# Optimization experiments

Measured on AMD Instinct MI355X. Metric: run time of the kernel, lower is better.

## Reference

```python
import jax, jax.numpy as jnp
import numpy as np

N_NODES = 50000
N_EDGES = 800000
IN_CH = 1024
OUT_CH = 256


def setup_inputs() -> dict:
    key = jax.random.key(0)
    ks = jax.random.split(key, 7)
    x = jax.random.normal(ks[0], (N_NODES, IN_CH), dtype=jnp.float32)
    src_index = jax.random.randint(ks[1], (N_EDGES,), 0, N_NODES, dtype=jnp.int32)
    tar_index = jax.random.randint(ks[2], (N_EDGES,), 0, N_NODES, dtype=jnp.int32)
    edge_weight = jax.random.uniform(ks[3], (N_EDGES,), dtype=jnp.float32)
    self_edge_weight = jax.random.uniform(ks[4], (N_NODES,), dtype=jnp.float32)
    # Linear layer params (torch.nn.Linear: y = x @ W.T + b)
    bound = 1.0 / np.sqrt(IN_CH)
    W = jax.random.uniform(ks[5], (OUT_CH, IN_CH), dtype=jnp.float32, minval=-bound, maxval=bound)
    b = jax.random.uniform(ks[6], (OUT_CH,), dtype=jnp.float32, minval=-bound, maxval=bound)
    return {"x": x, "W": W, "b": b, "src_index": src_index, "tar_index": tar_index,
            "edge_weight": edge_weight, "self_edge_weight": self_edge_weight}


def reference(x, W, b, src_index, tar_index, edge_weight, self_edge_weight):
    # dense linear projection: [N, in] -> [N, out]
    h = jnp.einsum('ni,oi->no', x, W) + b
    # edge aggregation: out[t] += w_e * h[src_e]  (SpMM-like gather/scatter)
    msgs = h[src_index] * edge_weight[:, None]          # [E, out]
    agg = jax.ops.segment_sum(msgs, tar_index, num_segments=h.shape[0])
    # self-loop term
    return agg + self_edge_weight[:, None] * h
```

## Files before the change

kernel.cpp:

```cpp
#include <hip/hip_runtime.h>
#include <hip/hip_bf16.h>

#define N_NODES 50000
#define N_EDGES 800000
#define IN_CH 1024
#define OUT_CH 256
#define NBLK 196

typedef __attribute__((ext_vector_type(8))) short bf16x8;
typedef __attribute__((ext_vector_type(4))) float f32x4;

__device__ inline unsigned short f2bf(float f) {
  union { float f; unsigned int u; } v; v.f = f;
  unsigned int r = v.u + 0x7fffu + ((v.u >> 16) & 1u);
  return (unsigned short)(r >> 16);
}
__device__ inline float bf2f(unsigned short u) {
  union { unsigned int u; float f; } v; v.u = ((unsigned int)u) << 16;
  return v.f;
}
__device__ inline unsigned int cvtpk_bf16(float a, float b) {
  unsigned int r;
  asm("v_cvt_pk_bf16_f32 %0, %1, %2" : "=v"(r) : "v"(a), "v"(b));
  return r;
}

#define GLOAD16(SRC, DST)                                                      \
  __builtin_amdgcn_global_load_lds(                                            \
      (const __attribute__((address_space(1))) void*)(SRC),                    \
      (__attribute__((address_space(3))) void*)(DST), 16, 0, 0)

__device__ inline void waitbar6() {
  __builtin_amdgcn_sched_barrier(0);
  asm volatile("s_waitcnt vmcnt(6)" ::: "memory");
  __builtin_amdgcn_s_barrier();
  __builtin_amdgcn_sched_barrier(0);
}
__device__ inline void waitbar0() {
  __builtin_amdgcn_sched_barrier(0);
  asm volatile("s_waitcnt vmcnt(0)" ::: "memory");
  __builtin_amdgcn_s_barrier();
  __builtin_amdgcn_sched_barrier(0);
}

__global__ __launch_bounds__(256) void prep_hist(const float* __restrict__ W,
                                                 unsigned short* __restrict__ Wb,
                                                 const int* __restrict__ tar,
                                                 int* __restrict__ counts) {
  const int b = blockIdx.x, t = threadIdx.x;
  if (b < 256) {
    const int i4 = (b * 256 + t) * 4;
    float4 f = *(const float4*)(W + i4);
    *(ushort4*)(Wb + i4) = make_ushort4(f2bf(f.x), f2bf(f.y), f2bf(f.z), f2bf(f.w));
  } else {
    const int e = (b - 256) * 256 + t;
    if (e < N_EDGES) atomicAdd(&counts[tar[e]], 1);
  }
}

__global__ __launch_bounds__(256, 2) void gemm_proj(
    const float* __restrict__ X, const unsigned short* __restrict__ Wb,
    const float* __restrict__ bias, unsigned short* __restrict__ Hb)
{
  __shared__ float lds_a[3][128][32];
  __shared__ unsigned short lds_b[3][128][32];

  const int tid  = threadIdx.x;
  const int lane = tid & 63;
  const int w    = tid >> 6;
  const int wr   = w >> 1, wc = w & 1;
  const int gm0  = blockIdx.x * 128;
  const int gn0  = blockIdx.y * 128;

  f32x4 acc[4][4];
  #pragma unroll
  for (int i = 0; i < 4; i++)
    #pragma unroll
    for (int j = 0; j < 4; j++) acc[i][j] = (f32x4)0.0f;

#define STAGE(BUF, K0)                                                         \
  {                                                                            \
    _Pragma("unroll")                                                          \
    for (int q = 0; q < 4; q++) {                                              \
      const int wl  = w * 4 + q;                                               \
      const int row = 8 * wl + (lane >> 3);                                    \
      int grow = gm0 + row;                                                    \
      if (grow > N_NODES - 1) grow = N_NODES - 1;                              \
      const int sc = (lane & 7) ^ (row & 7);                                   \
      GLOAD16(X + (size_t)grow * IN_CH + (K0) + sc * 4,                        \
              &lds_a[BUF][8 * wl][0]);                                         \
    }                                                                          \
    _Pragma("unroll")                                                          \
    for (int q = 0; q < 2; q++) {                                              \
      const int wl  = w * 2 + q;                                               \
      const int row = 16 * wl + (lane >> 2);                                   \
      const int sc  = (lane & 3) ^ (row & 3);                                  \
      GLOAD16(Wb + (size_t)(gn0 + row) * IN_CH + (K0) + sc * 8,                \
              &lds_b[BUF][16 * wl][0]);                                        \
    }                                                                          \
  }

#define COMPUTE(BUF)                                                           \
  {                                                                            \
    const int l15 = lane & 15;                                                 \
    const int kb  = lane >> 4;                                                 \
    bf16x8 af[4], bfr[4];                                                      \
    _Pragma("unroll")                                                          \
    for (int i = 0; i < 4; i++) {                                              \
      const int row = wr * 64 + i * 16 + l15;                                  \
      const int c0  = (2 * kb) ^ (row & 7);                                    \
      const int c1  = (2 * kb + 1) ^ (row & 7);                                \
      f32x4 lo = *(const f32x4*)&lds_a[BUF][row][c0 * 4];                      \
      f32x4 hi = *(const f32x4*)&lds_a[BUF][row][c1 * 4];                      \
      union { unsigned int u[4]; bf16x8 v; } t;                                \
      t.u[0] = cvtpk_bf16(lo[0], lo[1]);                                       \
      t.u[1] = cvtpk_bf16(lo[2], lo[3]);                                       \
      t.u[2] = cvtpk_bf16(hi[0], hi[1]);                                       \
      t.u[3] = cvtpk_bf16(hi[2], hi[3]);                                       \
      af[i] = t.v;                                                             \
    }                                                                          \
    _Pragma("unroll")                                                          \
    for (int j = 0; j < 4; j++) {                                              \
      const int row = wc * 64 + j * 16 + l15;                                  \
      const int c   = kb ^ (row & 3);                                          \
      bfr[j] = *(const bf16x8*)&lds_b[BUF][row][c * 8];                        \
    }                                                                          \
    _Pragma("unroll")                                                          \
    for (int i = 0; i < 4; i++)                                                \
      _Pragma("unroll")                                                        \
      for (int j = 0; j < 4; j++)                                              \
        acc[i][j] = __builtin_amdgcn_mfma_f32_16x16x32_bf16(af[i], bfr[j],     \
                                                            acc[i][j], 0, 0, 0); \
  }

  STAGE(0, 0);
  STAGE(1, 32);
  waitbar6();

  #pragma unroll
  for (int t = 0; t < 32; t++) {
    if (t + 2 < 32) STAGE((t + 2) % 3, (t + 2) * 32);
    COMPUTE(t % 3);
    if (t + 2 < 32)      waitbar6();
    else if (t == 30)    waitbar0();
  }
#undef STAGE
#undef COMPUTE

  float bj[4];
  #pragma unroll
  for (int j = 0; j < 4; j++)
    bj[j] = bias[gn0 + wc * 64 + j * 16 + (lane & 15)];

  #pragma unroll
  for (int i = 0; i < 4; i++) {
    const int grow_base = gm0 + wr * 64 + i * 16 + ((lane >> 4) << 2);
    #pragma unroll
    for (int r = 0; r < 4; r++) {
      const int grow = grow_base + r;
      if (grow < N_NODES) {
        #pragma unroll
        for (int j = 0; j < 4; j++) {
          const int gcol = gn0 + wc * 64 + j * 16 + (lane & 15);
          Hb[(size_t)grow * OUT_CH + gcol] = f2bf(acc[i][j][r] + bj[j]);
        }
      }
    }
  }
}

__global__ __launch_bounds__(256) void scan_block(const int* __restrict__ counts,
                                                  int* __restrict__ offsets,
                                                  int* __restrict__ blocksum) {
  __shared__ int wsum[4];
  const int tid = threadIdx.x, lane = tid & 63, wv = tid >> 6;
  const int i = blockIdx.x * 256 + tid;
  const int v = (i < N_NODES) ? counts[i] : 0;
  int s = v;
  #pragma unroll
  for (int off = 1; off < 64; off <<= 1) {
    int t = __shfl_up(s, off, 64);
    if (lane >= off) s += t;
  }
  if (lane == 63) wsum[wv] = s;
  __syncthreads();
  if (tid == 0) {
    int c = 0;
    #pragma unroll
    for (int k = 0; k < 4; k++) { int t = wsum[k]; wsum[k] = c; c += t; }
  }
  __syncthreads();
  const int excl = wsum[wv] + s - v;
  if (i < N_NODES) offsets[i] = excl;
  if (tid == 255) blocksum[blockIdx.x] = excl + v;
}

__global__ __launch_bounds__(256) void scan_sums(int* __restrict__ blocksum,
                                                 int* __restrict__ offsets) {
  __shared__ int wsum[4];
  const int tid = threadIdx.x, lane = tid & 63, wv = tid >> 6;
  const int v = (tid < NBLK) ? blocksum[tid] : 0;
  int s = v;
  #pragma unroll
  for (int off = 1; off < 64; off <<= 1) {
    int t = __shfl_up(s, off, 64);
    if (lane >= off) s += t;
  }
  if (lane == 63) wsum[wv] = s;
  __syncthreads();
  if (tid == 0) {
    int c = 0;
    #pragma unroll
    for (int k = 0; k < 4; k++) { int t = wsum[k]; wsum[k] = c; c += t; }
  }
  __syncthreads();
  const int excl = wsum[wv] + s - v;
  if (tid < NBLK) blocksum[tid] = excl;
  if (tid == 255) offsets[N_NODES] = excl;
}

__global__ __launch_bounds__(256) void finalize_offsets(int* __restrict__ offsets,
                                                        const int* __restrict__ blocksum,
                                                        int* __restrict__ cursor) {
  const int i = blockIdx.x * 256 + threadIdx.x;
  if (i < N_NODES) {
    const int off = offsets[i] + blocksum[i >> 8];
    offsets[i] = off;
    cursor[i] = off;
  }
}

__global__ __launch_bounds__(256) void fill_csr(const int* __restrict__ src,
                                                const int* __restrict__ tar,
                                                const float* __restrict__ ew,
                                                int* __restrict__ cursor,
                                                int2* __restrict__ edata) {
  int e = blockIdx.x * blockDim.x + threadIdx.x;
  if (e >= N_EDGES) return;
  const int t = tar[e];
  const int p = atomicAdd(&cursor[t], 1);
  edata[p] = make_int2(src[e], __float_as_int(ew[e]));
}

__global__ __launch_bounds__(256) void node_agg(
    const unsigned short* __restrict__ Hb, const int* __restrict__ offsets,
    const int2* __restrict__ edata, const float* __restrict__ sw,
    float* __restrict__ OUT)
{
  const int wid = (blockIdx.x * blockDim.x + threadIdx.x) >> 6;
  if (wid >= N_NODES) return;
  const int lane = threadIdx.x & 63;
  const int e0 = offsets[wid];
  const int e1 = offsets[wid + 1];

  float a0 = 0.f, a1 = 0.f, a2 = 0.f, a3 = 0.f;

  for (int base = e0; base < e1; base += 64) {
    const int avail = e1 - base;
    int2 d = make_int2(0, 0);
    if (lane < avail) d = edata[base + lane];
    const int n = (avail < 64) ? avail : 64;
    int j = 0;
    for (; j + 8 <= n; j += 8) {
      int   sE[8];
      float wE[8];
      #pragma unroll
      for (int q = 0; q < 8; q++) {
        sE[q] = __shfl(d.x, j + q, 64);
        wE[q] = __int_as_float(__shfl(d.y, j + q, 64));
      }
      ushort4 hE[8];
      #pragma unroll
      for (int q = 0; q < 8; q++)
        hE[q] = *(const ushort4*)(Hb + (size_t)sE[q] * OUT_CH + lane * 4);
      #pragma unroll
      for (int q = 0; q < 8; q++) {
        a0 += wE[q] * bf2f(hE[q].x);
        a1 += wE[q] * bf2f(hE[q].y);
        a2 += wE[q] * bf2f(hE[q].z);
        a3 += wE[q] * bf2f(hE[q].w);
      }
    }
    for (; j < n; j++) {
      const int   s = __shfl(d.x, j, 64);
      const float wgt = __int_as_float(__shfl(d.y, j, 64));
      const ushort4 h = *(const ushort4*)(Hb + (size_t)s * OUT_CH + lane * 4);
      a0 += wgt * bf2f(h.x); a1 += wgt * bf2f(h.y);
      a2 += wgt * bf2f(h.z); a3 += wgt * bf2f(h.w);
    }
  }

  const float swv = sw[wid];
  const ushort4 hs = *(const ushort4*)(Hb + (size_t)wid * OUT_CH + lane * 4);
  float4 o;
  o.x = a0 + swv * bf2f(hs.x);
  o.y = a1 + swv * bf2f(hs.y);
  o.z = a2 + swv * bf2f(hs.z);
  o.w = a3 + swv * bf2f(hs.w);
  *(float4*)(OUT + (size_t)wid * OUT_CH + lane * 4) = o;
}

extern "C" void kernel_launch(void* const* d_in, const int* in_sizes, int n_in,
                              void* d_out, int out_size, void* d_ws, size_t ws_size,
                              hipStream_t stream) {
  const float* x   = (const float*)d_in[0];
  const float* W   = (const float*)d_in[1];
  const float* b   = (const float*)d_in[2];
  const int*   src = (const int*)d_in[3];
  const int*   tar = (const int*)d_in[4];
  const float* ew  = (const float*)d_in[5];
  const float* sw  = (const float*)d_in[6];
  float* out = (float*)d_out;

  char* ws = (char*)d_ws;
  size_t o = 0;
  unsigned short* Wb = (unsigned short*)(ws + o);
  o += (size_t)OUT_CH * IN_CH * 2;          o = (o + 255) & ~(size_t)255;
  unsigned short* Hb = (unsigned short*)(ws + o);
  o += (size_t)N_NODES * OUT_CH * 2;        o = (o + 255) & ~(size_t)255;
  int* counts   = (int*)(ws + o); o += (size_t)N_NODES * 4;       o = (o + 255) & ~(size_t)255;
  int* offsets  = (int*)(ws + o); o += (size_t)(N_NODES + 1) * 4; o = (o + 255) & ~(size_t)255;
  int* cursor   = (int*)(ws + o); o += (size_t)N_NODES * 4;       o = (o + 255) & ~(size_t)255;
  int* blocksum = (int*)(ws + o); o += (size_t)NBLK * 4;          o = (o + 255) & ~(size_t)255;
  int2* edata   = (int2*)(ws + o);

  hipMemsetAsync(counts, 0, (size_t)N_NODES * 4, stream);
  prep_hist<<<256 + (N_EDGES + 255) / 256, 256, 0, stream>>>(W, Wb, tar, counts);
  scan_block<<<NBLK, 256, 0, stream>>>(counts, offsets, blocksum);
  scan_sums<<<1, 256, 0, stream>>>(blocksum, offsets);
  finalize_offsets<<<NBLK, 256, 0, stream>>>(offsets, blocksum, cursor);
  fill_csr<<<(N_EDGES + 255) / 256, 256, 0, stream>>>(src, tar, ew, cursor, edata);

  dim3 g1((N_NODES + 127) / 128, OUT_CH / 128);
  gemm_proj<<<g1, 256, 0, stream>>>(x, Wb, b, Hb);

  const long long nthreads = (long long)N_NODES * 64;
  node_agg<<<(int)((nthreads + 255) / 256), 256, 0, stream>>>(Hb, offsets, edata, sw, out);
}
```

Baseline: 236.3 us.

## Restructure projection GEMM to stream X through registers with full-width W tiles

The projection GEMM now gives each block 64 rows and all 256 output columns, so X is read from global memory once instead of twice across column tiles. A fragments are loaded straight from global into registers with a two-step register prefetch, while W chunks of 128 K-columns are staged in swizzled LDS via plain vector loads. This removes the async global-to-LDS copies of X and halves X traffic, at the cost of more accumulators per wave (16 MFMA tiles), synchronous W staging with barriers, and possibly lower occupancy.

Result: slower. 361.1 us (+52.8%).

```diff
diff --git a/kernel.cpp b/kernel.cpp
--- a/kernel.cpp
+++ b/kernel.cpp
@@ -25,20 +25,9 @@
   return r;
 }
 
-#define GLOAD16(SRC, DST)                                                      \
-  __builtin_amdgcn_global_load_lds(                                            \
-      (const __attribute__((address_space(1))) void*)(SRC),                    \
-      (__attribute__((address_space(3))) void*)(DST), 16, 0, 0)
-
-__device__ inline void waitbar6() {
+__device__ inline void barrier_nodrain() {
   __builtin_amdgcn_sched_barrier(0);
-  asm volatile("s_waitcnt vmcnt(6)" ::: "memory");
-  __builtin_amdgcn_s_barrier();
-  __builtin_amdgcn_sched_barrier(0);
-}
-__device__ inline void waitbar0() {
-  __builtin_amdgcn_sched_barrier(0);
-  asm volatile("s_waitcnt vmcnt(0)" ::: "memory");
+  asm volatile("s_waitcnt lgkmcnt(0)" ::: "memory");
   __builtin_amdgcn_s_barrier();
   __builtin_amdgcn_sched_barrier(0);
 }
@@ -62,109 +51,87 @@
     const float* __restrict__ X, const unsigned short* __restrict__ Wb,
     const float* __restrict__ bias, unsigned short* __restrict__ Hb)
 {
-  __shared__ float lds_a[3][128][32];
-  __shared__ unsigned short lds_b[3][128][32];
+  __shared__ unsigned short lds_w[256 * 128];
 
   const int tid  = threadIdx.x;
   const int lane = tid & 63;
-  const int w    = tid >> 6;
-  const int wr   = w >> 1, wc = w & 1;
-  const int gm0  = blockIdx.x * 128;
-  const int gn0  = blockIdx.y * 128;
-
-  f32x4 acc[4][4];
+  const int wv   = tid >> 6;
+  const int l15  = lane & 15;
+  const int hi   = lane >> 4;
+  const int m0   = blockIdx.x * 64;
+
+  const int  row = m0 + wv * 16 + l15;
+  const bool rok = row < N_NODES;
+  const float* xp = X + (size_t)row * IN_CH + hi * 8;
+  const float4 fz = make_float4(0.f, 0.f, 0.f, 0.f);
+
+  f32x4 acc[16];
   #pragma unroll
-  for (int i = 0; i < 4; i++)
+  for (int j = 0; j < 16; j++) acc[j] = (f32x4)0.0f;
+
+  const unsigned short* wsrc = Wb + (size_t)tid * IN_CH;
+  unsigned short* wdst = lds_w + tid * 128;
+  const int cxor = tid & 7;
+
+  float4 paA0, paA1, paB0, paB1;
+
+#define LOADA_A(KS) { const int k0_ = (KS) * 32;                               \
+    paA0 = rok ? *(const float4*)(xp + k0_)     : fz;                          \
+    paA1 = rok ? *(const float4*)(xp + k0_ + 4) : fz; }
+#define LOADA_B(KS) { const int k0_ = (KS) * 32;                               \
+    paB0 = rok ? *(const float4*)(xp + k0_)     : fz;                          \
+    paB1 = rok ? *(const float4*)(xp + k0_ + 4) : fz; }
+
+#define STEP(LK, KS, C0, C1, RELOAD)                                           \
+  {                                                                            \
+    const float4 ca0 = C0, ca1 = C1;                                           \
+    if ((KS) + 2 < 32) RELOAD((KS) + 2);                                       \
+    union { unsigned int u[4]; bf16x8 v; } t_;                                 \
+    t_.u[0] = cvtpk_bf16(ca0.x, ca0.y);                                        \
+    t_.u[1] = cvtpk_bf16(ca0.z, ca0.w);                                        \
+    t_.u[2] = cvtpk_bf16(ca1.x, ca1.y);                                        \
+    t_.u[3] = cvtpk_bf16(ca1.z, ca1.w);                                        \
+    const int phys_ = (((LK) << 2) + hi) ^ (l15 & 7);                          \
+    _Pragma("unroll")                                                          \
+    for (int j = 0; j < 16; j++) {                                             \
+      const bf16x8 bf =                                                        \
+          *(const bf16x8*)&lds_w[(j * 16 + l15) * 128 + phys_ * 8];            \
+      acc[j] = __builtin_amdgcn_mfma_f32_16x16x32_bf16(t_.v, bf, acc[j],       \
+                                                       0, 0, 0);               \
+    }                                                                          \
+  }
+
+  LOADA_A(0);
+  LOADA_B(1);
+
+  for (int kc = 0; kc < 8; kc++) {
+    if (kc) barrier_nodrain();
     #pragma unroll
-    for (int j = 0; j < 4; j++) acc[i][j] = (f32x4)0.0f;
-
-#define STAGE(BUF, K0)                                                         \
-  {                                                                            \
-    _Pragma("unroll")                                                          \
-    for (int q = 0; q < 4; q++) {                                              \
-      const int wl  = w * 4 + q;                                               \
-      const int row = 8 * wl + (lane >> 3);                                    \
-      int grow = gm0 + row;                                                    \
-      if (grow > N_NODES - 1) grow = N_NODES - 1;                              \
-      const int sc = (lane & 7) ^ (row & 7);                                   \
-      GLOAD16(X + (size_t)grow * IN_CH + (K0) + sc * 4,                        \
-              &lds_a[BUF][8 * wl][0]);                                         \
-    }                                                                          \
-    _Pragma("unroll")                                                          \
-    for (int q = 0; q < 2; q++) {                                              \
-      const int wl  = w * 2 + q;                                               \
-      const int row = 16 * wl + (lane >> 2);                                   \
-      const int sc  = (lane & 3) ^ (row & 3);                                  \
-      GLOAD16(Wb + (size_t)(gn0 + row) * IN_CH + (K0) + sc * 8,                \
-              &lds_b[BUF][16 * wl][0]);                                        \
-    }                                                                          \
-  }
-
-#define COMPUTE(BUF)                                                           \
-  {                                                                            \
-    const int l15 = lane & 15;                                                 \
-    const int kb  = lane >> 4;                                                 \
-    bf16x8 af[4], bfr[4];                                                      \
-    _Pragma("unroll")                                                          \
-    for (int i = 0; i < 4; i++) {                                              \
-      const int row = wr * 64 + i * 16 + l15;                                  \
-      const int c0  = (2 * kb) ^ (row & 7);                                    \
-      const int c1  = (2 * kb + 1) ^ (row & 7);                                \
-      f32x4 lo = *(const f32x4*)&lds_a[BUF][row][c0 * 4];                      \
-      f32x4 hi = *(const f32x4*)&lds_a[BUF][row][c1 * 4];                      \
-      union { unsigned int u[4]; bf16x8 v; } t;                                \
-      t.u[0] = cvtpk_bf16(lo[0], lo[1]);                                       \
-      t.u[1] = cvtpk_bf16(lo[2], lo[3]);                                       \
-      t.u[2] = cvtpk_bf16(hi[0], hi[1]);                                       \
-      t.u[3] = cvtpk_bf16(hi[2], hi[3]);                                       \
-      af[i] = t.v;                                                             \
-    }                                                                          \
-    _Pragma("unroll")                                                          \
-    for (int j = 0; j < 4; j++) {                                              \
-      const int row = wc * 64 + j * 16 + l15;                                  \
-      const int c   = kb ^ (row & 3);                                          \
-      bfr[j] = *(const bf16x8*)&lds_b[BUF][row][c * 8];                        \
-    }                                                                          \
-    _Pragma("unroll")                                                          \
-    for (int i = 0; i < 4; i++)                                                \
-      _Pragma("unroll")                                                        \
-      for (int j = 0; j < 4; j++)                                              \
-        acc[i][j] = __builtin_amdgcn_mfma_f32_16x16x32_bf16(af[i], bfr[j],     \
-                                                            acc[i][j], 0, 0, 0); \
-  }
-
-  STAGE(0, 0);
-  STAGE(1, 32);
-  waitbar6();
+    for (int c = 0; c < 16; c++) {
+      const bf16x8 v = *(const bf16x8*)(wsrc + kc * 128 + c * 8);
+      *(bf16x8*)(wdst + (c ^ cxor) * 8) = v;
+    }
+    barrier_nodrain();
+
+    const int ks0 = kc * 4;
+    STEP(0, ks0 + 0, paA0, paA1, LOADA_A);
+    STEP(1, ks0 + 1, paB0, paB1, LOADA_B);
+    STEP(2, ks0 + 2, paA0, paA1, LOADA_A);
+    STEP(3, ks0 + 3, paB0, paB1, LOADA_B);
+  }
+#undef LOADA_A
+#undef LOADA_B
+#undef STEP
 
   #pragma unroll
-  for (int t = 0; t < 32; t++) {
-    if (t + 2 < 32) STAGE((t + 2) % 3, (t + 2) * 32);
-    COMPUTE(t % 3);
-    if (t + 2 < 32)      waitbar6();
-    else if (t == 30)    waitbar0();
-  }
-#undef STAGE
-#undef COMPUTE
-
-  float bj[4];
-  #pragma unroll
-  for (int j = 0; j < 4; j++)
-    bj[j] = bias[gn0 + wc * 64 + j * 16 + (lane & 15)];
-
-  #pragma unroll
-  for (int i = 0; i < 4; i++) {
-    const int grow_base = gm0 + wr * 64 + i * 16 + ((lane >> 4) << 2);
+  for (int j = 0; j < 16; j++) {
+    const int gcol = j * 16 + l15;
+    const float bj = bias[gcol];
     #pragma unroll
     for (int r = 0; r < 4; r++) {
-      const int grow = grow_base + r;
-      if (grow < N_NODES) {
-        #pragma unroll
-        for (int j = 0; j < 4; j++) {
-          const int gcol = gn0 + wc * 64 + j * 16 + (lane & 15);
-          Hb[(size_t)grow * OUT_CH + gcol] = f2bf(acc[i][j][r] + bj[j]);
-        }
-      }
+      const int grow = m0 + wv * 16 + hi * 4 + r;
+      if (grow < N_NODES)
+        Hb[(size_t)grow * OUT_CH + gcol] = f2bf(acc[j][r] + bj);
     }
   }
 }
@@ -331,7 +298,7 @@
   finalize_offsets<<<NBLK, 256, 0, stream>>>(offsets, blocksum, cursor);
   fill_csr<<<(N_EDGES + 255) / 256, 256, 0, stream>>>(src, tar, ew, cursor, edata);
 
-  dim3 g1((N_NODES + 127) / 128, OUT_CH / 128);
+  dim3 g1((N_NODES + 63) / 64);
   gemm_proj<<<g1, 256, 0, stream>>>(x, Wb, b, Hb);
 
   const long long nthreads = (long long)N_NODES * 64;
```
